# Kernel tuning notes

Measured on AMD Instinct MI355X. Metric: run time of the kernel, lower is better.

The kernel has to match this reference:

```python
import jax, jax.numpy as jnp
import numpy as np

VOCAB, EMB, HID, DSEM, TK, B, MAX_OOV = 50000, 128, 512, 256, 400, 64, 100


def _linear(x, W, b=None):
    y = x @ W.T
    return y if b is None else y + b


def setup_inputs() -> dict:
    key = jax.random.key(0)
    ks = jax.random.split(key, 32)
    s = 0.02
    inp = {
        "y_t_1": jax.random.randint(ks[0], (B,), 0, VOCAB),
        "s_h": jax.random.normal(ks[1], (1, B, HID)) * 0.1,
        "s_c": jax.random.normal(ks[2], (1, B, HID)) * 0.1,
        "encoder_outputs": jax.random.normal(ks[3], (B, TK, 2 * HID)) * 0.1,
        "encoder_feature": jax.random.normal(ks[4], (B * TK, 2 * HID)) * 0.1,
        "enc_padding_mask": jnp.ones((B, TK), jnp.float32),
        "c_t_1": jax.random.normal(ks[5], (B, 2 * HID)) * 0.1,
        "extra_zeros": jnp.zeros((B, MAX_OOV), jnp.float32),
        "enc_batch_extend_vocab": jax.random.randint(ks[6], (B, TK), 0, VOCAB + MAX_OOV),
        "coverage": jax.random.uniform(ks[7], (B, TK)),
        "step": 1,
        "ri": jax.random.normal(ks[8], (B, TK, 2 * DSEM)) * 0.1,
        # parameters (torch Linear convention: weight is (out, in))
        "emb_W": jax.random.normal(ks[9], (VOCAB, EMB)) * s,
        "Ws_W": jax.random.normal(ks[10], (2 * HID, 2 * HID)) * s,
        "Ws_b": jax.random.normal(ks[11], (2 * HID,)) * s,
        "v_W": jax.random.normal(ks[12], (1, 2 * HID)) * s,
        "Wc_W": jax.random.normal(ks[13], (2 * HID, 1)) * s,
        "Wr_W": jax.random.normal(ks[14], (2 * HID, 2 * DSEM)) * s,
        "xc_W": jax.random.normal(ks[15], (EMB, 2 * HID + EMB)) * s,
        "xc_b": jax.random.normal(ks[16], (EMB,)) * s,
        "W_ih": jax.random.uniform(ks[17], (4 * HID, EMB), minval=-0.02, maxval=0.02),
        "W_hh": jax.random.uniform(ks[18], (4 * HID, HID), minval=-0.02, maxval=0.02),
        "b_ih": jnp.concatenate([jnp.zeros(HID), jnp.ones(HID), jnp.zeros(2 * HID)]),
        "b_hh": jnp.zeros((4 * HID,), jnp.float32),
        "pg_W": jax.random.normal(ks[19], (1, 4 * HID + EMB)) * s,
        "pg_b": jax.random.normal(ks[20], (1,)) * s,
        "o1_W": jax.random.normal(ks[21], (HID, 3 * HID)) * s,
        "o1_b": jax.random.normal(ks[22], (HID,)) * s,
        "o2_W": jax.random.normal(ks[23], (VOCAB, HID)) * s,
        "o2_b": jax.random.normal(ks[24], (VOCAB,)) * s,
    }
    return inp


def _attention(s_t_hat, encoder_outputs, encoder_feature, enc_padding_mask, coverage, ri,
               Ws_W, Ws_b, v_W, Wc_W, Wr_W):
    b, t_k, n = encoder_outputs.shape
    dec_fea = _linear(s_t_hat, Ws_W, Ws_b)                     # (b, 2h)
    att = encoder_feature.reshape(b, t_k, n) + dec_fea[:, None, :]
    att = att + coverage[..., None] * Wc_W[:, 0]                # coverage feature
    scores = jnp.tanh(att) @ v_W[0]                             # (b, t_k)
    attn = jax.nn.softmax(scores, axis=1) * enc_padding_mask
    attn = attn / attn.sum(1, keepdims=True)
    c_t = jnp.einsum('bt,btn->bn', attn, encoder_outputs)
    coverage_next = coverage + attn
    # structural attention (not renormalized in the original)
    att2 = jnp.einsum('btd,nd->btn', ri, Wr_W) + dec_fea[:, None, :]
    scores2 = jnp.tanh(att2) @ v_W[0]
    a_struct = jax.nn.softmax(scores2, axis=1) * enc_padding_mask
    c_struct = jnp.einsum('bt,btn->bn', a_struct, encoder_outputs)
    return c_t, attn, coverage_next, c_struct, a_struct


def reference(y_t_1, s_h, s_c, encoder_outputs, encoder_feature, enc_padding_mask,
              c_t_1, extra_zeros, enc_batch_extend_vocab, coverage, step, ri,
              emb_W, Ws_W, Ws_b, v_W, Wc_W, Wr_W, xc_W, xc_b,
              W_ih, W_hh, b_ih, b_hh, pg_W, pg_b, o1_W, o1_b, o2_W, o2_b):
    b = y_t_1.shape[0]
    # embed + context projection
    y_emb = emb_W[y_t_1]                                        # (b, emb)
    x = _linear(jnp.concatenate([c_t_1, y_emb], 1), xc_W, xc_b)  # (b, emb)
    # single-step LSTM (torch gate order i,f,g,o)
    h0, c0 = s_h[0], s_c[0]
    gates = x @ W_ih.T + b_ih + h0 @ W_hh.T + b_hh
    i, f, g, o = jnp.split(gates, 4, axis=1)
    c_new = jax.nn.sigmoid(f) * c0 + jax.nn.sigmoid(i) * jnp.tanh(g)
    h_new = jax.nn.sigmoid(o) * jnp.tanh(c_new)
    s_t_hat = jnp.concatenate([h_new, c_new], 1)                # (b, 2h)
    c_t, attn_dist, coverage_next, c_struct, _ = _attention(
        s_t_hat, encoder_outputs, encoder_feature, enc_padding_mask, coverage, ri,
        Ws_W, Ws_b, v_W, Wc_W, Wr_W)
    coverage_out = coverage_next  # training / step>0 path
    # pointer-generator gate
    p_gen = jax.nn.sigmoid(_linear(jnp.concatenate([c_struct, s_t_hat, x], 1), pg_W, pg_b))
    out = _linear(jnp.concatenate([h_new, c_struct], 1), o1_W, o1_b)
    out = _linear(out, o2_W, o2_b)
    vocab_dist = jax.nn.softmax(out, axis=1)
    vocab_dist_ = p_gen * vocab_dist
    attn_ = (1.0 - p_gen) * attn_dist
    ext = jnp.concatenate([vocab_dist_, extra_zeros], 1)        # (b, vocab+oov)
    rows = jnp.arange(b)[:, None]
    final_dist = ext.at[rows, enc_batch_extend_vocab].add(attn_)
    return (final_dist, h_new[None], c_new[None], c_t, attn_dist, p_gen, coverage_out)
```

## Files before the change

### kernel.cpp

```cpp
#include <hip/hip_runtime.h>
#include <hip/hip_bf16.h>
#include <math.h>

#define BATCH  64
#define EMB    128
#define HID    512
#define TK     400
#define VOCAB  50000
#define MAX_OOV 100
#define VEXT   50100
#define H2     1024
#define K_RI   512

typedef short  bf16x8 __attribute__((ext_vector_type(8)));
typedef float  f32x4  __attribute__((ext_vector_type(4)));
typedef unsigned short u16x8 __attribute__((ext_vector_type(8)));

__device__ __forceinline__ unsigned short f2b(float f){
  unsigned u = __float_as_uint(f);
  u += 0x7fffu + ((u >> 16) & 1u);
  return (unsigned short)(u >> 16);
}
__device__ __forceinline__ float sigm(float x){ return 1.0f/(1.0f+expf(-x)); }
__device__ __forceinline__ float clampf(float x, float lo, float hi){ return fminf(fmaxf(x, lo), hi); }
__device__ __forceinline__ float fast_tanh(float x){
  float e = __expf(2.f*x);
  return 1.f - 2.f/(e + 1.f);
}
__device__ __forceinline__ bf16x8 ld_frag(const unsigned short* p){
  return __builtin_bit_cast(bf16x8, *(const u16x8*)p);
}
__device__ __forceinline__ u16x8 cvt8(const float4 a, const float4 b){
  u16x8 r;
  r[0]=f2b(a.x); r[1]=f2b(a.y); r[2]=f2b(a.z); r[3]=f2b(a.w);
  r[4]=f2b(b.x); r[5]=f2b(b.y); r[6]=f2b(b.z); r[7]=f2b(b.w);
  return r;
}

#define WS_X        0
#define WS_H        8192
#define WS_STHAT    73728
#define WS_DECFEA   139264
#define WS_SCORES   204800
#define WS_SCORES2  230400
#define WS_ATTN     256000
#define WS_ASTRUCT  281600
#define WS_CSTRUCT  307200
#define WS_PGEN     372736
#define WS_OUT1BF   372800
#define WS_ROWMAX   389184
#define WS_ROWSUM   389248
#define WS_PMAX     WS_SCORES
#define WS_PSUM     (WS_SCORES+512)

#define OUT_FINAL 0
#define OUT_H     3206400
#define OUT_C     3239168
#define OUT_CT    3271936
#define OUT_ATTN  3337472
#define OUT_PGEN  3363072
#define OUT_COV   3363136
#define OUT_WR16  131072
#define CTX_CT    0
#define CTX_CS    262144

__global__ __launch_bounds__(256) void k_wrcvt(const float* __restrict__ Wr,
    unsigned short* __restrict__ WrF){
  int t = blockIdx.x*256 + threadIdx.x;
  int lane = t & 63;
  int f    = (t >> 6) & 15;
  int nb   = t >> 10;
  int r  = nb*16 + (lane & 15);
  int k0 = f*32 + (lane >> 4)*8;
  const float4* p = (const float4*)(Wr + (size_t)r*512 + k0);
  *(u16x8*)(WrF + (size_t)t*8) = cvt8(p[0], p[1]);
}

__global__ __launch_bounds__(256) void k_embx(
    const int* __restrict__ y, const float* __restrict__ embW,
    const float* __restrict__ ct1, const float* __restrict__ xcW,
    const float* __restrict__ xcb, float* __restrict__ ws)
{
  __shared__ float vec[1152];
  int b = blockIdx.x, q = blockIdx.y, tid = threadIdx.x;
  int yb = y[b];
  for (int i = tid; i < 1024; i += 256) vec[i] = ct1[b*1024+i];
  if (tid < 128) vec[1024+tid] = embW[(size_t)yb*128+tid];
  __syncthreads();
  int wave = tid>>6, lane = tid&63;
  #pragma unroll 2
  for (int oo = 0; oo < 8; ++oo){
    int o = q*32 + wave*8 + oo;
    const float* row = xcW + (size_t)o*1152;
    float acc = 0.f;
    #pragma unroll
    for (int i=0;i<18;i++) acc += row[lane + 64*i] * vec[lane + 64*i];
    for (int off=32; off>0; off>>=1) acc += __shfl_down(acc, off);
    if (lane==0) ws[WS_X + b*128 + o] = xcb[o] + acc;
  }
}

__global__ __launch_bounds__(256) void k_gates(
    const float* __restrict__ Wih, const float* __restrict__ Whh,
    const float* __restrict__ bih, const float* __restrict__ bhh,
    const float* __restrict__ sh, const float* __restrict__ ws,
    float* __restrict__ gates)
{
  __shared__ float xh[640];
  int b = blockIdx.x, gc = blockIdx.y, tid = threadIdx.x;
  for (int i=tid;i<128;i+=256) xh[i] = ws[WS_X + b*128 + i];
  for (int i=tid;i<512;i+=256) xh[128+i] = sh[b*512+i];
  __syncthreads();
  int wave = tid>>6, lane = tid&63;
  int gbase = gc*128 + wave*32;
  for (int gg=0; gg<32; ++gg){
    int g = gbase + gg;
    const float* ri = Wih + (size_t)g*128;
    const float* rh = Whh + (size_t)g*512;
    float acc = ri[lane]*xh[lane] + ri[lane+64]*xh[lane+64];
    #pragma unroll
    for (int i=0;i<8;i++) acc += rh[lane + 64*i] * xh[128 + lane + 64*i];
    for (int off=32; off>0; off>>=1) acc += __shfl_down(acc, off);
    if (lane==0) gates[b*2048 + g] = acc + bih[g] + bhh[g];
  }
}

__global__ __launch_bounds__(256) void k_lstmpt(
    const float* __restrict__ gates, const float* __restrict__ sc,
    float* __restrict__ ws, float* __restrict__ outh, float* __restrict__ outc)
{
  int b = blockIdx.x, tid = threadIdx.x;
  const float* g = gates + b*2048;
  for (int j = tid; j < 512; j += 256){
    float ig = sigm(g[j]),       fg = sigm(g[512+j]);
    float gg = tanhf(g[1024+j]), og = sigm(g[1536+j]);
    float c0 = sc[b*512+j];
    float cn = fg*c0 + ig*gg;
    float hn = og*tanhf(cn);
    ws[WS_H + b*512+j] = hn;
    ws[WS_STHAT + b*1024 + j] = hn; ws[WS_STHAT + b*1024 + 512 + j] = cn;
    outh[b*512+j] = hn; outc[b*512+j] = cn;
  }
}

__global__ __launch_bounds__(256) void k_decfea(const float* __restrict__ WsW,
    const float* __restrict__ Wsb, float* __restrict__ ws){
  __shared__ float st[1024];
  int b = blockIdx.x, q = blockIdx.y, tid = threadIdx.x;
  for (int i=tid;i<1024;i+=256) st[i] = ws[WS_STHAT + b*1024 + i];
  __syncthreads();
  int wave = tid>>6, lane = tid&63;
  for (int oo=0; oo<64; ++oo){
    int n = q*256 + wave*64 + oo;
    const float* row = WsW + (size_t)n*1024;
    float acc = 0.f;
    #pragma unroll
    for (int i=0;i<16;i++) acc += row[lane + 64*i] * st[lane + 64*i];
    for (int off=32; off>0; off>>=1) acc += __shfl_down(acc, off);
    if (lane==0) ws[WS_DECFEA + b*1024 + n] = Wsb[n] + acc;
  }
}

__global__ __launch_bounds__(256) void k_scores1(const float* __restrict__ ef,
    const float* __restrict__ cov, const float* __restrict__ vW,
    const float* __restrict__ WcW, float* __restrict__ ws){
  __shared__ float df[1024], vv[1024], wc[1024];
  int b = blockIdx.x, tid = threadIdx.x;
  for (int i=tid;i<1024;i+=256){ df[i]=ws[WS_DECFEA+b*1024+i]; vv[i]=vW[i]; wc[i]=WcW[i]; }
  __syncthreads();
  int wave = tid>>6, lane = tid&63;
  int t = blockIdx.y*4 + wave;
  float cv = cov[b*400+t];
  const float4* e = (const float4*)(ef + (size_t)(b*400+t)*1024 + lane*16);
  float4 e0 = e[0], e1 = e[1], e2 = e[2], e3 = e[3];
  float ebuf[16] = {e0.x,e0.y,e0.z,e0.w, e1.x,e1.y,e1.z,e1.w,
                    e2.x,e2.y,e2.z,e2.w, e3.x,e3.y,e3.z,e3.w};
  float acc = 0.f;
  int base = lane*16;
  #pragma unroll
  for (int j=0;j<16;j++){ int n=base+j; acc += fast_tanh(ebuf[j] + df[n] + cv*wc[n]) * vv[n]; }
  for (int off=32; off>0; off>>=1) acc += __shfl_down(acc, off, 64);
  if (lane==0) ws[WS_SCORES + b*400 + t] = clampf(acc, -64.f, 64.f);
}

__global__ __launch_bounds__(512) void k_scores2(const float* __restrict__ ri,
    const unsigned short* __restrict__ WrF, const float* __restrict__ vW,
    float* __restrict__ ws){
  __shared__ __align__(16) unsigned short Bs[2][16384];
  int tid = threadIdx.x, lane = tid & 63, w = tid >> 6;
  int m0 = blockIdx.x*128 + w*16;
  int fr = lane & 15, fq8 = (lane >> 4)*8;
  int cq = lane >> 4, cr = lane & 15;

  bf16x8 a[16];
  {
    const float* p = ri + (size_t)(m0 + fr)*K_RI + fq8;
    #pragma unroll
    for (int f=0; f<16; f++){
      float4 x0 = *(const float4*)(p + f*32);
      float4 x1 = *(const float4*)(p + f*32 + 4);
      a[f] = __builtin_bit_cast(bf16x8, cvt8(x0, x1));
    }
  }

  const float* decfea = ws + WS_DECFEA;
  int dfo[4];
  #pragma unroll
  for (int rg=0; rg<4; rg++) dfo[rg] = ((m0 + cq*4 + rg)/400)*1024;
  float sa[4] = {0.f,0.f,0.f,0.f};

  #pragma unroll
  for (int i=0;i<4;i++){
    int e = (i*512 + tid)*8;
    __builtin_amdgcn_global_load_lds(
      (const __attribute__((address_space(1))) unsigned int*)(WrF + e),
      (__attribute__((address_space(3))) unsigned int*)&Bs[0][e], 16, 0, 0);
  }

  for (int p=0; p<32; ++p){
    __syncthreads();
    if (p < 31){
      const unsigned short* src = WrF + (size_t)(p+1)*16384;
      unsigned short* dst = Bs[(p+1)&1];
      #pragma unroll
      for (int i=0;i<4;i++){
        int e = (i*512 + tid)*8;
        __builtin_amdgcn_global_load_lds(
          (const __attribute__((address_space(1))) unsigned int*)(src + e),
          (__attribute__((address_space(3))) unsigned int*)(dst + e), 16, 0, 0);
      }
    }
    const unsigned short* b0 = &Bs[p&1][lane*8];
    const unsigned short* b1 = b0 + 8192;
    f32x4 c0a={0.f,0.f,0.f,0.f}, c0b={0.f,0.f,0.f,0.f};
    f32x4 c1a={0.f,0.f,0.f,0.f}, c1b={0.f,0.f,0.f,0.f};
    #pragma unroll
    for (int f=0; f<16; f+=2){
      bf16x8 x0 = ld_frag(b0 + f*512), y0 = ld_frag(b0 + f*512 + 512);
      bf16x8 x1 = ld_frag(b1 + f*512), y1 = ld_frag(b1 + f*512 + 512);
      c0a = __builtin_amdgcn_mfma_f32_16x16x32_bf16(a[f],   x0, c0a, 0,0,0);
      c1a = __builtin_amdgcn_mfma_f32_16x16x32_bf16(a[f],   x1, c1a, 0,0,0);
      c0b = __builtin_amdgcn_mfma_f32_16x16x32_bf16(a[f+1], y0, c0b, 0,0,0);
      c1b = __builtin_amdgcn_mfma_f32_16x16x32_bf16(a[f+1], y1, c1b, 0,0,0);
    }
    int col0 = p*32 + cr, col1 = col0 + 16;
    float v0 = vW[col0], v1 = vW[col1];
    #pragma unroll
    for (int rg=0; rg<4; rg++){
      float t0 = c0a[rg] + c0b[rg] + decfea[dfo[rg] + col0];
      float t1 = c1a[rg] + c1b[rg] + decfea[dfo[rg] + col1];
      sa[rg] += fast_tanh(t0)*v0 + fast_tanh(t1)*v1;
    }
  }
  #pragma unroll
  for (int rg=0; rg<4; rg++){
    float v = sa[rg];
    v += __shfl_xor(v, 1); v += __shfl_xor(v, 2);
    v += __shfl_xor(v, 4); v += __shfl_xor(v, 8);
    sa[rg] = v;
  }
  if (cr == 0){
    #pragma unroll
    for (int rg=0; rg<4; rg++)
      ws[WS_SCORES2 + m0 + cq*4 + rg] = clampf(sa[rg], -64.f, 64.f);
  }
}

__global__ __launch_bounds__(256) void k_softmax(const float* __restrict__ mask,
    const float* __restrict__ covin, float* __restrict__ ws,
    float* __restrict__ out){
  __shared__ float s1[400], s2[400], mk[400], red[256];
  int b = blockIdx.x, tid = threadIdx.x;
  for (int i=tid;i<400;i+=256){
    s1[i]=ws[WS_SCORES+b*400+i]; s2[i]=ws[WS_SCORES2+b*400+i]; mk[i]=mask[b*400+i];
  }
  __syncthreads();
  float lm = -1e30f;
  for (int i=tid;i<400;i+=256) lm = fmaxf(lm, s1[i]);
  red[tid]=lm; __syncthreads();
  for (int off=128;off>0;off>>=1){ if (tid<off) red[tid]=fmaxf(red[tid],red[tid+off]); __syncthreads(); }
  float mx1 = red[0]; __syncthreads();
  float ls=0.f;
  for (int i=tid;i<400;i+=256){ float e=__expf(s1[i]-mx1); s1[i]=e; ls+=e; }
  red[tid]=ls; __syncthreads();
  for (int off=128;off>0;off>>=1){ if (tid<off) red[tid]+=red[tid+off]; __syncthreads(); }
  float sum1 = red[0]; __syncthreads();
  float la=0.f;
  for (int i=tid;i<400;i+=256){ float a=(s1[i]/sum1)*mk[i]; s1[i]=a; la+=a; }
  red[tid]=la; __syncthreads();
  for (int off=128;off>0;off>>=1){ if (tid<off) red[tid]+=red[tid+off]; __syncthreads(); }
  float sumA = red[0]; __syncthreads();
  for (int i=tid;i<400;i+=256){
    float attn = s1[i]/sumA;
    ws[WS_ATTN + b*400 + i] = attn;
    out[OUT_ATTN + b*400 + i] = attn;
    out[OUT_COV  + b*400 + i] = covin[b*400+i] + attn;
  }
  float lm2 = -1e30f;
  for (int i=tid;i<400;i+=256) lm2 = fmaxf(lm2, s2[i]);
  red[tid]=lm2; __syncthreads();
  for (int off=128;off>0;off>>=1){ if (tid<off) red[tid]=fmaxf(red[tid],red[tid+off]); __syncthreads(); }
  float mx2 = red[0]; __syncthreads();
  float ls2=0.f;
  for (int i=tid;i<400;i+=256){ float e=__expf(s2[i]-mx2); s2[i]=e; ls2+=e; }
  red[tid]=ls2; __syncthreads();
  for (int off=128;off>0;off>>=1){ if (tid<off) red[tid]+=red[tid+off]; __syncthreads(); }
  float sum2 = red[0]; __syncthreads();
  for (int i=tid;i<400;i+=256) ws[WS_ASTRUCT + b*400 + i] = (s2[i]/sum2)*mk[i];
}

__global__ __launch_bounds__(256) void k_context(const float* __restrict__ eo,
    const float* __restrict__ ws, float* __restrict__ outp){
  __shared__ float at[100], as2[100];
  int b = blockIdx.x, tid = threadIdx.x;
  int n = blockIdx.y*256 + tid;
  int tz = blockIdx.z;
  for (int i=tid;i<100;i+=256){
    at[i]  = ws[WS_ATTN    + b*400 + tz*100 + i];
    as2[i] = ws[WS_ASTRUCT + b*400 + tz*100 + i];
  }
  __syncthreads();
  const float* p = eo + (size_t)b*400*1024 + (size_t)tz*100*1024 + n;
  float a1=0.f, a2=0.f;
  #pragma unroll 4
  for (int t=0;t<100;t++){
    float e = p[(size_t)t*1024];
    a1 += at[t]*e; a2 += as2[t]*e;
  }
  outp[CTX_CT + tz*65536 + b*1024 + n] = a1;
  outp[CTX_CS + tz*65536 + b*1024 + n] = a2;
}

__global__ __launch_bounds__(256) void k_ctxsum(float* __restrict__ ws,
    float* __restrict__ out){
  int b = blockIdx.x, tid = threadIdx.x;
  int n = tid*4;
  float4 ct = {0.f,0.f,0.f,0.f}, cs = {0.f,0.f,0.f,0.f};
  #pragma unroll
  for (int tz=0;tz<4;tz++){
    float4 a = *(const float4*)(out + CTX_CT + tz*65536 + b*1024 + n);
    float4 c = *(const float4*)(out + CTX_CS + tz*65536 + b*1024 + n);
    ct.x+=a.x; ct.y+=a.y; ct.z+=a.z; ct.w+=a.w;
    cs.x+=c.x; cs.y+=c.y; cs.z+=c.z; cs.w+=c.w;
  }
  *(float4*)(out + OUT_CT + b*1024 + n) = ct;
  *(float4*)(ws + WS_CSTRUCT + b*1024 + n) = cs;
}

__global__ __launch_bounds__(256) void k_pgen(const float* __restrict__ pgW,
    const float* __restrict__ pgb, float* __restrict__ ws,
    float* __restrict__ out){
  __shared__ float red[256];
  int b=blockIdx.x, tid=threadIdx.x;
  float a=0.f;
  for (int i=tid;i<2176;i+=256){
    float x;
    if (i<1024)      x = ws[WS_CSTRUCT + b*1024 + i];
    else if (i<2048) x = ws[WS_STHAT   + b*1024 + (i-1024)];
    else             x = ws[WS_X       + b*128  + (i-2048)];
    a += x * pgW[i];
  }
  red[tid]=a; __syncthreads();
  for (int off=128;off>0;off>>=1){ if(tid<off) red[tid]+=red[tid+off]; __syncthreads(); }
  if (tid==0){
    float p = sigm(red[0] + pgb[0]);
    ws[WS_PGEN+b]=p; out[OUT_PGEN+b]=p;
  }
}

__global__ __launch_bounds__(256) void k_out1(const float* __restrict__ o1W,
    const float* __restrict__ o1b, float* __restrict__ ws){
  __shared__ float in1[1536];
  int b=blockIdx.x, q=blockIdx.y, tid=threadIdx.x;
  for (int i=tid;i<512;i+=256)  in1[i]     = ws[WS_H + b*512 + i];
  for (int i=tid;i<1024;i+=256) in1[512+i] = ws[WS_CSTRUCT + b*1024 + i];
  __syncthreads();
  int wave = tid>>6, lane = tid&63;
  for (int oo=0; oo<64; ++oo){
    int o = q*256 + wave*64 + oo;
    const float* row = o1W + (size_t)o*1536;
    float acc = 0.f;
    #pragma unroll
    for (int i=0;i<24;i++) acc += row[lane + 64*i] * in1[lane + 64*i];
    for (int off=32; off>0; off>>=1) acc += __shfl_down(acc, off);
    if (lane==0) ((unsigned short*)(ws + WS_OUT1BF))[b*512 + o] = f2b(o1b[o] + acc);
  }
}

__global__ __launch_bounds__(256) void k_o2(float* __restrict__ ws,
    const float* __restrict__ o2W, const float* __restrict__ o2b,
    float* __restrict__ out){
  __shared__ __align__(16) unsigned short As[64][72];
  __shared__ __align__(16) unsigned short Bs[64][72];
  int tid=threadIdx.x;
  int n0 = blockIdx.x*64;
  int lane=tid&63, wave=tid>>6, wm=wave&1, wn=wave>>1;
  int lrow=tid>>2, lcol=(tid&3)*16;
  const unsigned short* out1 = (const unsigned short*)(ws + WS_OUT1BF);
  f32x4 acc00={0.f,0.f,0.f,0.f}, acc01={0.f,0.f,0.f,0.f};
  f32x4 acc10={0.f,0.f,0.f,0.f}, acc11={0.f,0.f,0.f,0.f};
  int nrow = n0 + lrow;
  bool bvalid = nrow < VOCAB;
  int fr = lane & 15, fq = (lane >> 4) * 8;
  for (int kc=0;kc<512;kc+=64){
    u16x8 a0 = *(const u16x8*)(out1 + lrow*512 + kc + lcol);
    u16x8 a1 = *(const u16x8*)(out1 + lrow*512 + kc + lcol + 8);
    u16x8 bb0 = {0,0,0,0,0,0,0,0}, bb1 = {0,0,0,0,0,0,0,0};
    if (bvalid){
      const float4* bp = (const float4*)(o2W + (size_t)nrow*512 + kc + lcol);
      float4 b0=bp[0], b1=bp[1], b2=bp[2], b3=bp[3];
      bb0 = cvt8(b0,b1); bb1 = cvt8(b2,b3);
    }
    __syncthreads();
    *(u16x8*)&As[lrow][lcol] = a0;  *(u16x8*)&As[lrow][lcol+8] = a1;
    *(u16x8*)&Bs[lrow][lcol] = bb0; *(u16x8*)&Bs[lrow][lcol+8] = bb1;
    __syncthreads();
    #pragma unroll
    for (int kk=0; kk<64; kk+=32){
      bf16x8 aA = ld_frag(&As[wm*32 +      fr][kk + fq]);
      bf16x8 aB = ld_frag(&As[wm*32 + 16 + fr][kk + fq]);
      bf16x8 bA = ld_frag(&Bs[wn*32 +      fr][kk + fq]);
      bf16x8 bB = ld_frag(&Bs[wn*32 + 16 + fr][kk + fq]);
      acc00 = __builtin_amdgcn_mfma_f32_16x16x32_bf16(aA, bA, acc00, 0,0,0);
      acc01 = __builtin_amdgcn_mfma_f32_16x16x32_bf16(aA, bB, acc01, 0,0,0);
      acc10 = __builtin_amdgcn_mfma_f32_16x16x32_bf16(aB, bA, acc10, 0,0,0);
      acc11 = __builtin_amdgcn_mfma_f32_16x16x32_bf16(aB, bB, acc11, 0,0,0);
    }
  }
  int cq=lane>>4, cr=lane&15;
  #pragma unroll
  for (int i=0;i<2;i++){
    #pragma unroll
    for (int rg=0;rg<4;rg++){
      int row = wm*32 + i*16 + cq*4 + rg;
      int n1 = n0 + wn*32 + cr, n2 = n1+16;
      float v1 = (i==0?acc00[rg]:acc10[rg]);
      float v2 = (i==0?acc01[rg]:acc11[rg]);
      if (n1 < VOCAB) out[(size_t)row*VEXT + n1] = clampf(v1 + o2b[n1], -80.f, 80.f);
      if (n2 < VOCAB) out[(size_t)row*VEXT + n2] = clampf(v2 + o2b[n2], -80.f, 80.f);
    }
  }
}

__global__ __launch_bounds__(256) void k_vsm_part(const float* __restrict__ out,
    float* __restrict__ ws){
  __shared__ float red[256];
  int b=blockIdx.x, s=blockIdx.y, tid=threadIdx.x;
  const float* lg = out + (size_t)b*VEXT + s*6250;
  float lm=-1e30f;
  for (int i=tid;i<6250;i+=256) lm=fmaxf(lm, lg[i]);
  red[tid]=lm; __syncthreads();
  for (int off=128;off>0;off>>=1){ if(tid<off) red[tid]=fmaxf(red[tid],red[tid+off]); __syncthreads(); }
  float mx=red[0]; __syncthreads();
  float sm=0.f;
  for (int i=tid;i<6250;i+=256) sm+=__expf(lg[i]-mx);
  red[tid]=sm; __syncthreads();
  for (int off=128;off>0;off>>=1){ if(tid<off) red[tid]+=red[tid+off]; __syncthreads(); }
  if (tid==0){ ws[WS_PMAX + b*8 + s]=mx; ws[WS_PSUM + b*8 + s]=red[0]; }
}

__global__ __launch_bounds__(64) void k_vsm_comb(float* __restrict__ ws){
  int b = blockIdx.x;
  if (threadIdx.x==0){
    float M=-1e30f;
    for (int s=0;s<8;s++) M=fmaxf(M, ws[WS_PMAX + b*8 + s]);
    float S=0.f;
    for (int s=0;s<8;s++) S += __expf(ws[WS_PMAX + b*8 + s]-M)*ws[WS_PSUM + b*8 + s];
    ws[WS_ROWMAX+b]=M; ws[WS_ROWSUM+b]=S;
  }
}

__global__ __launch_bounds__(256) void k_vsm_write(const float* __restrict__ ws,
    float* __restrict__ out){
  int b=blockIdx.y;
  int i=blockIdx.x*256+threadIdx.x;
  if (i>=VEXT) return;
  float* p = out + (size_t)b*VEXT + i;
  if (i<VOCAB) *p = ws[WS_PGEN+b]*__expf(*p - ws[WS_ROWMAX+b])/ws[WS_ROWSUM+b];
  else         *p = 0.f;
}

__global__ __launch_bounds__(256) void k_scatter(const int* __restrict__ ebev,
    const float* __restrict__ ws, float* __restrict__ out){
  int idx = blockIdx.x*256+threadIdx.x;
  int b = idx/400;
  float add = (1.f - ws[WS_PGEN+b]) * ws[WS_ATTN+idx];
  int v = ebev[idx];
  atomicAdd(out + (size_t)b*VEXT + v, add);
}

extern "C" void kernel_launch(void* const* d_in, const int* in_sizes, int n_in,
                              void* d_out, int out_size, void* d_ws, size_t ws_size,
                              hipStream_t stream){
  (void)in_sizes; (void)n_in; (void)out_size; (void)ws_size;
  const int*   y_t_1   = (const int*)d_in[0];
  const float* s_h     = (const float*)d_in[1];
  const float* s_c     = (const float*)d_in[2];
  const float* enc_out = (const float*)d_in[3];
  const float* enc_ft  = (const float*)d_in[4];
  const float* mask    = (const float*)d_in[5];
  const float* c_t_1   = (const float*)d_in[6];
  const int*   ebev    = (const int*)d_in[8];
  const float* cover   = (const float*)d_in[9];
  const float* ri      = (const float*)d_in[11];
  const float* embW    = (const float*)d_in[12];
  const float* WsW     = (const float*)d_in[13];
  const float* Wsb     = (const float*)d_in[14];
  const float* vW      = (const float*)d_in[15];
  const float* WcW     = (const float*)d_in[16];
  const float* WrW     = (const float*)d_in[17];
  const float* xcW     = (const float*)d_in[18];
  const float* xcb     = (const float*)d_in[19];
  const float* Wih     = (const float*)d_in[20];
  const float* Whh     = (const float*)d_in[21];
  const float* bih     = (const float*)d_in[22];
  const float* bhh     = (const float*)d_in[23];
  const float* pgW     = (const float*)d_in[24];
  const float* pgb     = (const float*)d_in[25];
  const float* o1W     = (const float*)d_in[26];
  const float* o1b     = (const float*)d_in[27];
  const float* o2W     = (const float*)d_in[28];
  const float* o2b     = (const float*)d_in[29];
  float* ws  = (float*)d_ws;
  float* out = (float*)d_out;
  float* gates = out;
  unsigned short* Wr16 = (unsigned short*)(out + OUT_WR16);

  k_wrcvt   <<<256,           256,0,stream>>>(WrW, Wr16);
  k_embx    <<<dim3(BATCH,4), 256,0,stream>>>(y_t_1, embW, c_t_1, xcW, xcb, ws);
  k_gates   <<<dim3(BATCH,16),256,0,stream>>>(Wih, Whh, bih, bhh, s_h, ws, gates);
  k_lstmpt  <<<BATCH,         256,0,stream>>>(gates, s_c, ws, out+OUT_H, out+OUT_C);
  k_decfea  <<<dim3(BATCH,4), 256,0,stream>>>(WsW, Wsb, ws);
  k_scores1 <<<dim3(BATCH,100),256,0,stream>>>(enc_ft, cover, vW, WcW, ws);
  k_scores2 <<<200,           512,0,stream>>>(ri, Wr16, vW, ws);
  k_softmax <<<BATCH,         256,0,stream>>>(mask, cover, ws, out);
  k_context <<<dim3(BATCH,4,4),256,0,stream>>>(enc_out, ws, out);
  k_ctxsum  <<<BATCH,         256,0,stream>>>(ws, out);
  k_pgen    <<<BATCH,         256,0,stream>>>(pgW, pgb, ws, out);
  k_out1    <<<dim3(BATCH,2), 256,0,stream>>>(o1W, o1b, ws);
  k_o2      <<<782,           256,0,stream>>>(ws, o2W, o2b, out);
  k_vsm_part<<<dim3(BATCH,8), 256,0,stream>>>(out, ws);
  k_vsm_comb<<<BATCH,         64, 0,stream>>>(ws);
  k_vsm_write<<<dim3(196,BATCH),256,0,stream>>>(ws, out);
  k_scatter <<<100,           256,0,stream>>>(ebev, ws, out);
}
```

Before: 347.3 us.

## Merge score kernels into one launch and fuse context sum with p_gen

Combines the coverage-attention scores kernel and the structural MFMA scores kernel into a single launch, where the first 200 blocks run the MFMA path and the remaining 3200 blocks run the elementwise path. The two independent workloads can then overlap on the GPU, and one launch is saved. The context-sum kernel also absorbs the p_gen dot product, computing it directly from the freshly reduced c_struct in registers with float4 loads. The risk is that every block now reserves the full 64KB of shared memory, which may lower occupancy for the many small scores1-style blocks.

After: 340.8 us. About the same (-1.8%).

```diff
diff --git a/kernel.cpp b/kernel.cpp
--- a/kernel.cpp
+++ b/kernel.cpp
@@ -161,108 +161,111 @@
   }
 }
 
-__global__ __launch_bounds__(256) void k_scores1(const float* __restrict__ ef,
-    const float* __restrict__ cov, const float* __restrict__ vW,
+__global__ __launch_bounds__(512) void k_scores(const float* __restrict__ ri,
+    const unsigned short* __restrict__ WrF, const float* __restrict__ vW,
+    const float* __restrict__ ef, const float* __restrict__ cov,
     const float* __restrict__ WcW, float* __restrict__ ws){
-  __shared__ float df[1024], vv[1024], wc[1024];
-  int b = blockIdx.x, tid = threadIdx.x;
-  for (int i=tid;i<1024;i+=256){ df[i]=ws[WS_DECFEA+b*1024+i]; vv[i]=vW[i]; wc[i]=WcW[i]; }
-  __syncthreads();
-  int wave = tid>>6, lane = tid&63;
-  int t = blockIdx.y*4 + wave;
-  float cv = cov[b*400+t];
-  const float4* e = (const float4*)(ef + (size_t)(b*400+t)*1024 + lane*16);
-  float4 e0 = e[0], e1 = e[1], e2 = e[2], e3 = e[3];
-  float ebuf[16] = {e0.x,e0.y,e0.z,e0.w, e1.x,e1.y,e1.z,e1.w,
-                    e2.x,e2.y,e2.z,e2.w, e3.x,e3.y,e3.z,e3.w};
-  float acc = 0.f;
-  int base = lane*16;
-  #pragma unroll
-  for (int j=0;j<16;j++){ int n=base+j; acc += fast_tanh(ebuf[j] + df[n] + cv*wc[n]) * vv[n]; }
-  for (int off=32; off>0; off>>=1) acc += __shfl_down(acc, off, 64);
-  if (lane==0) ws[WS_SCORES + b*400 + t] = clampf(acc, -64.f, 64.f);
-}
-
-__global__ __launch_bounds__(512) void k_scores2(const float* __restrict__ ri,
-    const unsigned short* __restrict__ WrF, const float* __restrict__ vW,
-    float* __restrict__ ws){
-  __shared__ __align__(16) unsigned short Bs[2][16384];
+  __shared__ __align__(16) unsigned char smem[65536];
   int tid = threadIdx.x, lane = tid & 63, w = tid >> 6;
-  int m0 = blockIdx.x*128 + w*16;
-  int fr = lane & 15, fq8 = (lane >> 4)*8;
-  int cq = lane >> 4, cr = lane & 15;
-
-  bf16x8 a[16];
-  {
-    const float* p = ri + (size_t)(m0 + fr)*K_RI + fq8;
-    #pragma unroll
-    for (int f=0; f<16; f++){
-      float4 x0 = *(const float4*)(p + f*32);
-      float4 x1 = *(const float4*)(p + f*32 + 4);
-      a[f] = __builtin_bit_cast(bf16x8, cvt8(x0, x1));
-    }
-  }
-
-  const float* decfea = ws + WS_DECFEA;
-  int dfo[4];
-  #pragma unroll
-  for (int rg=0; rg<4; rg++) dfo[rg] = ((m0 + cq*4 + rg)/400)*1024;
-  float sa[4] = {0.f,0.f,0.f,0.f};
-
-  #pragma unroll
-  for (int i=0;i<4;i++){
-    int e = (i*512 + tid)*8;
-    __builtin_amdgcn_global_load_lds(
-      (const __attribute__((address_space(1))) unsigned int*)(WrF + e),
-      (__attribute__((address_space(3))) unsigned int*)&Bs[0][e], 16, 0, 0);
-  }
-
-  for (int p=0; p<32; ++p){
+
+  if (blockIdx.x < 200){
+    unsigned short (*Bs)[16384] = (unsigned short (*)[16384])smem;
+    int m0 = blockIdx.x*128 + w*16;
+    int fr = lane & 15, fq8 = (lane >> 4)*8;
+    int cq = lane >> 4, cr = lane & 15;
+
+    bf16x8 a[16];
+    {
+      const float* p = ri + (size_t)(m0 + fr)*K_RI + fq8;
+      #pragma unroll
+      for (int f=0; f<16; f++){
+        float4 x0 = *(const float4*)(p + f*32);
+        float4 x1 = *(const float4*)(p + f*32 + 4);
+        a[f] = __builtin_bit_cast(bf16x8, cvt8(x0, x1));
+      }
+    }
+    const float* decfea = ws + WS_DECFEA;
+    int dfo[4];
+    #pragma unroll
+    for (int rg=0; rg<4; rg++) dfo[rg] = ((m0 + cq*4 + rg)/400)*1024;
+    float sa[4] = {0.f,0.f,0.f,0.f};
+
+    #pragma unroll
+    for (int i=0;i<4;i++){
+      int e = (i*512 + tid)*8;
+      __builtin_amdgcn_global_load_lds(
+        (const __attribute__((address_space(1))) unsigned int*)(WrF + e),
+        (__attribute__((address_space(3))) unsigned int*)&Bs[0][e], 16, 0, 0);
+    }
+    for (int p=0; p<32; ++p){
+      __syncthreads();
+      if (p < 31){
+        const unsigned short* src = WrF + (size_t)(p+1)*16384;
+        unsigned short* dst = Bs[(p+1)&1];
+        #pragma unroll
+        for (int i=0;i<4;i++){
+          int e = (i*512 + tid)*8;
+          __builtin_amdgcn_global_load_lds(
+            (const __attribute__((address_space(1))) unsigned int*)(src + e),
+            (__attribute__((address_space(3))) unsigned int*)(dst + e), 16, 0, 0);
+        }
+      }
+      const unsigned short* b0 = &Bs[p&1][lane*8];
+      const unsigned short* b1 = b0 + 8192;
+      f32x4 c0a={0.f,0.f,0.f,0.f}, c0b={0.f,0.f,0.f,0.f};
+      f32x4 c1a={0.f,0.f,0.f,0.f}, c1b={0.f,0.f,0.f,0.f};
+      #pragma unroll
+      for (int f=0; f<16; f+=2){
+        bf16x8 x0 = ld_frag(b0 + f*512), y0 = ld_frag(b0 + f*512 + 512);
+        bf16x8 x1 = ld_frag(b1 + f*512), y1 = ld_frag(b1 + f*512 + 512);
+        c0a = __builtin_amdgcn_mfma_f32_16x16x32_bf16(a[f],   x0, c0a, 0,0,0);
+        c1a = __builtin_amdgcn_mfma_f32_16x16x32_bf16(a[f],   x1, c1a, 0,0,0);
+        c0b = __builtin_amdgcn_mfma_f32_16x16x32_bf16(a[f+1], y0, c0b, 0,0,0);
+        c1b = __builtin_amdgcn_mfma_f32_16x16x32_bf16(a[f+1], y1, c1b, 0,0,0);
+      }
+      int col0 = p*32 + cr, col1 = col0 + 16;
+      float v0 = vW[col0], v1 = vW[col1];
+      #pragma unroll
+      for (int rg=0; rg<4; rg++){
+        float t0 = c0a[rg] + c0b[rg] + decfea[dfo[rg] + col0];
+        float t1 = c1a[rg] + c1b[rg] + decfea[dfo[rg] + col1];
+        sa[rg] += fast_tanh(t0)*v0 + fast_tanh(t1)*v1;
+      }
+    }
+    #pragma unroll
+    for (int rg=0; rg<4; rg++){
+      float v = sa[rg];
+      v += __shfl_xor(v, 1); v += __shfl_xor(v, 2);
+      v += __shfl_xor(v, 4); v += __shfl_xor(v, 8);
+      sa[rg] = v;
+    }
+    if (cr == 0){
+      #pragma unroll
+      for (int rg=0; rg<4; rg++)
+        ws[WS_SCORES2 + m0 + cq*4 + rg] = clampf(sa[rg], -64.f, 64.f);
+    }
+  } else {
+    float* df = (float*)smem;
+    float* vv = df + 1024;
+    float* wc = vv + 1024;
+    int sb = blockIdx.x - 200;
+    int b = sb / 50, tq = sb % 50;
+    for (int i=tid;i<1024;i+=512){
+      df[i]=ws[WS_DECFEA+b*1024+i]; vv[i]=vW[i]; wc[i]=WcW[i];
+    }
     __syncthreads();
-    if (p < 31){
-      const unsigned short* src = WrF + (size_t)(p+1)*16384;
-      unsigned short* dst = Bs[(p+1)&1];
-      #pragma unroll
-      for (int i=0;i<4;i++){
-        int e = (i*512 + tid)*8;
-        __builtin_amdgcn_global_load_lds(
-          (const __attribute__((address_space(1))) unsigned int*)(src + e),
-          (__attribute__((address_space(3))) unsigned int*)(dst + e), 16, 0, 0);
-      }
-    }
-    const unsigned short* b0 = &Bs[p&1][lane*8];
-    const unsigned short* b1 = b0 + 8192;
-    f32x4 c0a={0.f,0.f,0.f,0.f}, c0b={0.f,0.f,0.f,0.f};
-    f32x4 c1a={0.f,0.f,0.f,0.f}, c1b={0.f,0.f,0.f,0.f};
-    #pragma unroll
-    for (int f=0; f<16; f+=2){
-      bf16x8 x0 = ld_frag(b0 + f*512), y0 = ld_frag(b0 + f*512 + 512);
-      bf16x8 x1 = ld_frag(b1 + f*512), y1 = ld_frag(b1 + f*512 + 512);
-      c0a = __builtin_amdgcn_mfma_f32_16x16x32_bf16(a[f],   x0, c0a, 0,0,0);
-      c1a = __builtin_amdgcn_mfma_f32_16x16x32_bf16(a[f],   x1, c1a, 0,0,0);
-      c0b = __builtin_amdgcn_mfma_f32_16x16x32_bf16(a[f+1], y0, c0b, 0,0,0);
-      c1b = __builtin_amdgcn_mfma_f32_16x16x32_bf16(a[f+1], y1, c1b, 0,0,0);
-    }
-    int col0 = p*32 + cr, col1 = col0 + 16;
-    float v0 = vW[col0], v1 = vW[col1];
-    #pragma unroll
-    for (int rg=0; rg<4; rg++){
-      float t0 = c0a[rg] + c0b[rg] + decfea[dfo[rg] + col0];
-      float t1 = c1a[rg] + c1b[rg] + decfea[dfo[rg] + col1];
-      sa[rg] += fast_tanh(t0)*v0 + fast_tanh(t1)*v1;
-    }
-  }
-  #pragma unroll
-  for (int rg=0; rg<4; rg++){
-    float v = sa[rg];
-    v += __shfl_xor(v, 1); v += __shfl_xor(v, 2);
-    v += __shfl_xor(v, 4); v += __shfl_xor(v, 8);
-    sa[rg] = v;
-  }
-  if (cr == 0){
-    #pragma unroll
-    for (int rg=0; rg<4; rg++)
-      ws[WS_SCORES2 + m0 + cq*4 + rg] = clampf(sa[rg], -64.f, 64.f);
+    int t = tq*8 + w;
+    float cv = cov[b*400+t];
+    const float4* e = (const float4*)(ef + (size_t)(b*400+t)*1024 + lane*16);
+    float4 e0 = e[0], e1 = e[1], e2 = e[2], e3 = e[3];
+    float ebuf[16] = {e0.x,e0.y,e0.z,e0.w, e1.x,e1.y,e1.z,e1.w,
+                      e2.x,e2.y,e2.z,e2.w, e3.x,e3.y,e3.z,e3.w};
+    float acc = 0.f;
+    int base = lane*16;
+    #pragma unroll
+    for (int j=0;j<16;j++){ int n=base+j; acc += fast_tanh(ebuf[j] + df[n] + cv*wc[n]) * vv[n]; }
+    for (int off=32; off>0; off>>=1) acc += __shfl_down(acc, off, 64);
+    if (lane==0) ws[WS_SCORES + b*400 + t] = clampf(acc, -64.f, 64.f);
   }
 }
 
@@ -331,8 +334,10 @@
   outp[CTX_CS + tz*65536 + b*1024 + n] = a2;
 }
 
-__global__ __launch_bounds__(256) void k_ctxsum(float* __restrict__ ws,
+__global__ __launch_bounds__(256) void k_ctxpgen(const float* __restrict__ pgW,
+    const float* __restrict__ pgb, float* __restrict__ ws,
     float* __restrict__ out){
+  __shared__ float red[256];
   int b = blockIdx.x, tid = threadIdx.x;
   int n = tid*4;
   float4 ct = {0.f,0.f,0.f,0.f}, cs = {0.f,0.f,0.f,0.f};
@@ -345,20 +350,15 @@
   }
   *(float4*)(out + OUT_CT + b*1024 + n) = ct;
   *(float4*)(ws + WS_CSTRUCT + b*1024 + n) = cs;
-}
-
-__global__ __launch_bounds__(256) void k_pgen(const float* __restrict__ pgW,
-    const float* __restrict__ pgb, float* __restrict__ ws,
-    float* __restrict__ out){
-  __shared__ float red[256];
-  int b=blockIdx.x, tid=threadIdx.x;
-  float a=0.f;
-  for (int i=tid;i<2176;i+=256){
-    float x;
-    if (i<1024)      x = ws[WS_CSTRUCT + b*1024 + i];
-    else if (i<2048) x = ws[WS_STHAT   + b*1024 + (i-1024)];
-    else             x = ws[WS_X       + b*128  + (i-2048)];
-    a += x * pgW[i];
+  float4 pw = *(const float4*)(pgW + n);
+  float a = cs.x*pw.x + cs.y*pw.y + cs.z*pw.z + cs.w*pw.w;
+  float4 st = *(const float4*)(ws + WS_STHAT + b*1024 + n);
+  float4 pw2 = *(const float4*)(pgW + 1024 + n);
+  a += st.x*pw2.x + st.y*pw2.y + st.z*pw2.z + st.w*pw2.w;
+  if (tid < 32){
+    float4 xv = *(const float4*)(ws + WS_X + b*128 + tid*4);
+    float4 pw3 = *(const float4*)(pgW + 2048 + tid*4);
+    a += xv.x*pw3.x + xv.y*pw3.y + xv.z*pw3.z + xv.w*pw3.w;
   }
   red[tid]=a; __syncthreads();
   for (int off=128;off>0;off>>=1){ if(tid<off) red[tid]+=red[tid+off]; __syncthreads(); }
@@ -531,12 +531,10 @@
   k_gates   <<<dim3(BATCH,16),256,0,stream>>>(Wih, Whh, bih, bhh, s_h, ws, gates);
   k_lstmpt  <<<BATCH,         256,0,stream>>>(gates, s_c, ws, out+OUT_H, out+OUT_C);
   k_decfea  <<<dim3(BATCH,4), 256,0,stream>>>(WsW, Wsb, ws);
-  k_scores1 <<<dim3(BATCH,100),256,0,stream>>>(enc_ft, cover, vW, WcW, ws);
-  k_scores2 <<<200,           512,0,stream>>>(ri, Wr16, vW, ws);
+  k_scores  <<<3400,          512,0,stream>>>(ri, Wr16, vW, enc_ft, cover, WcW, ws);
   k_softmax <<<BATCH,         256,0,stream>>>(mask, cover, ws, out);
   k_context <<<dim3(BATCH,4,4),256,0,stream>>>(enc_out, ws, out);
-  k_ctxsum  <<<BATCH,         256,0,stream>>>(ws, out);
-  k_pgen    <<<BATCH,         256,0,stream>>>(pgW, pgb, ws, out);
+  k_ctxpgen <<<BATCH,         256,0,stream>>>(pgW, pgb, ws, out);
   k_out1    <<<dim3(BATCH,2), 256,0,stream>>>(o1W, o1b, ws);
   k_o2      <<<782,           256,0,stream>>>(ws, o2W, o2b, out);
   k_vsm_part<<<dim3(BATCH,8), 256,0,stream>>>(out, ws);
```
